# Kernel optimization log

Measured on AMD Instinct MI355X. Metric: run time of the kernel, lower is better.

Reference implementation:

```python
import jax, jax.numpy as jnp
import numpy as np

K = 32  # neighbors per query point


def _gather_points(x, idx):
    # x: [B, N, D], idx: [B, M, k] -> [B, M, k, D]
    B, M, k = idx.shape
    D = x.shape[-1]
    flat = jnp.take_along_axis(x, idx.reshape(B, M * k, 1), axis=1)
    return flat.reshape(B, M, k, D)


def setup_inputs() -> dict:
    key = jax.random.key(0)
    k1, k2, k3, k4, k5 = jax.random.split(key, 5)
    B, N, M, Cin = 16, 4096, 1024, 64
    pos = jax.random.normal(k1, (B, N, 3), dtype=jnp.float32)
    features = jax.random.normal(k2, (B, N, Cin), dtype=jnp.float32)
    idx = jax.random.randint(k3, (B, M), 0, N, dtype=jnp.int64)
    # 1x1 conv2d MLP params: (Cin+3) -> 64 -> 128 (use_xyz adds 3 channels)
    W1 = jax.random.normal(k4, (Cin + 3, 64), dtype=jnp.float32) * (1.0 / np.sqrt(Cin + 3))
    b1 = jnp.zeros((64,), dtype=jnp.float32)
    W2 = jax.random.normal(k5, (64, 128), dtype=jnp.float32) * (1.0 / np.sqrt(64))
    b2 = jnp.zeros((128,), dtype=jnp.float32)
    return {"pos": pos, "features": features, "W1": W1, "b1": b1,
            "W2": W2, "b2": b2, "idx": idx}


def reference(pos, features, W1, b1, W2, b2, idx):
    # pos: [B,N,3], features: [B,N,C], idx: [B,M] query-point indices
    pos_q = jnp.take_along_axis(pos, idx[..., None], axis=1)  # [B,M,3]
    # squared-distance knn: [B,M,N]
    d2 = (jnp.sum(pos_q ** 2, -1, keepdims=True)
          + jnp.sum(pos ** 2, -1)[:, None, :]
          - 2.0 * jnp.einsum("bmd,bnd->bmn", pos_q, pos))
    _, nn_idx = jax.lax.top_k(-d2, K)  # [B,M,K] nearest neighbors
    grouped_pos = _gather_points(pos, nn_idx)          # [B,M,K,3]
    grouped_feat = _gather_points(features, nn_idx)    # [B,M,K,C]
    rel = grouped_pos - pos_q[:, :, None, :]           # recenter groups
    x = jnp.concatenate([rel, grouped_feat], axis=-1)  # [B,M,K,C+3] (use_xyz)
    # 1x1 conv2d MLP == per-point linear + ReLU on channel dim
    h = jax.nn.relu(jnp.einsum("bmkc,cd->bmkd", x, W1) + b1)
    h = jax.nn.relu(jnp.einsum("bmkc,cd->bmkd", h, W2) + b2)
    out = jnp.max(h, axis=-2)  # max over K neighbors -> [B,M,128]
    return (pos_q, out)
```

## Files before the change

kernel.cpp:

```cpp
#include <hip/hip_runtime.h>

#define NPTS  4096
#define MQ    1024
#define BATCH 16
#define KNN   32
#define CIN   64
#define H1D   64
#define H2D   128

typedef _Float16 half8 __attribute__((ext_vector_type(8)));
typedef float    floatx4 __attribute__((ext_vector_type(4)));

#define WS_NN_BYTES ((size_t)BATCH * MQ * KNN * 4)
#define W1F_HALVES  (3 * 4 * 64 * 8)
#define W2F_HALVES  (2 * 8 * 64 * 8)
#define WS_PP_OFF   (WS_NN_BYTES + (W1F_HALVES + W2F_HALVES) * 2)

__global__ __launch_bounds__(256) void wprep_kernel(
    const float* __restrict__ W1, const float* __restrict__ W2,
    const float* __restrict__ pos,
    _Float16* __restrict__ wout, float* __restrict__ pp)
{
    const int gid = blockIdx.x * 256 + threadIdx.x;
    if (gid < 768) {
        const int s = gid;
        const int kc = s >> 8, nt = (s >> 6) & 3, lane = s & 63;
        const int col = lane & 15, quad = lane >> 4;
        half8 ph;
#pragma unroll
        for (int j = 0; j < 8; ++j) {
            const int k = kc * 32 + quad * 8 + j;
            ph[j] = (k < 67) ? (_Float16)W1[k * H1D + nt * 16 + col] : (_Float16)0.0f;
        }
        *(half8*)(wout + (size_t)s * 8) = ph;
    } else if (gid < 1792) {
        const int s2 = gid - 768;
        const int kc2 = s2 >> 9, nt2 = (s2 >> 6) & 7, lane = s2 & 63;
        const int col = lane & 15, quad = lane >> 4;
        half8 ph;
#pragma unroll
        for (int j = 0; j < 8; ++j) {
            const int k = kc2 * 32 + quad * 8 + j;
            ph[j] = (_Float16)W2[k * H2D + nt2 * 16 + col];
        }
        *(half8*)(wout + (size_t)W1F_HALVES + (size_t)s2 * 8) = ph;
    } else {
        const int p = gid - 1792;
        if (p < BATCH * NPTS) {
            const float px = pos[p * 3 + 0], py = pos[p * 3 + 1], pz = pos[p * 3 + 2];
            pp[p] = __fadd_rn(__fadd_rn(__fmul_rn(px, px), __fmul_rn(py, py)),
                              __fmul_rn(pz, pz));
        }
    }
}

__global__ __launch_bounds__(256) void knn_kernel(
    const float* __restrict__ pos, const float* __restrict__ pp,
    const int* __restrict__ idx,
    float* __restrict__ pos_q, int* __restrict__ nn)
{
    const int bid = blockIdx.x;
    const int b   = bid >> 10;
    const int m   = bid & (MQ - 1);
    const int t   = threadIdx.x;
    const int wv  = t >> 6, lane = t & 63;

    __shared__ unsigned int keys[NPTS];
    __shared__ unsigned int hist[2048];
    __shared__ unsigned int wsum[4];
    __shared__ unsigned int sc[8];
    __shared__ unsigned int ckey[64];
    __shared__ int          cidx[64];
    __shared__ int          outidx[KNN];

    const float* pb  = pos + (size_t)b * NPTS * 3;
    const float* ppb = pp + (size_t)b * NPTS;
    const int qn = idx[(size_t)b * MQ + m];
    const float qx = pb[qn * 3 + 0], qy = pb[qn * 3 + 1], qz = pb[qn * 3 + 2];
    const float qq = ppb[qn];

    for (int i = 0; i < NPTS / 256; ++i) {
        const int n = i * 256 + t;
        const float px = pb[n * 3 + 0], py = pb[n * 3 + 1], pz = pb[n * 3 + 2];
        const float qp = __fadd_rn(__fadd_rn(__fmul_rn(qx, px), __fmul_rn(qy, py)),
                                   __fmul_rn(qz, pz));
        const float d2 = __fsub_rn(__fadd_rn(qq, ppb[n]), __fmul_rn(2.0f, qp));
        unsigned int u = __float_as_uint(d2);
        u = (u & 0x80000000u) ? ~u : (u | 0x80000000u);
        keys[n] = u;
    }

    unsigned int prefix = 0u, rank = KNN - 1;
    int shift = 21, bcnt = NPTS;
    for (int level = 0; level < 3; ++level) {
        shift = (level == 0) ? 21 : (level == 1) ? 10 : 0;
        const int nb = (level < 2) ? 11 : 10;
        const int nbins = 1 << nb;
        const unsigned int mask = nbins - 1;
        const int hs = shift + nb;
        for (int j = t; j < nbins; j += 256) hist[j] = 0u;
        __syncthreads();
        for (int i = 0; i < NPTS / 256; ++i) {
            const unsigned int u = keys[i * 256 + t];
            if (level == 0 || (u >> hs) == prefix)
                atomicAdd(&hist[(u >> shift) & mask], 1u);
        }
        __syncthreads();
        const int g = nbins >> 8;
        unsigned int s = 0;
        for (int j = 0; j < g; ++j) s += hist[t * g + j];
        unsigned int v = s;
#pragma unroll
        for (int off = 1; off < 64; off <<= 1) {
            const unsigned int o = __shfl_up(v, off);
            if (lane >= off) v += o;
        }
        if (lane == 63) wsum[wv] = v;
        __syncthreads();
        unsigned int woff = 0;
        for (int i = 0; i < wv; ++i) woff += wsum[i];
        const unsigned int incl = woff + v, excl = incl - s;
        if (s > 0 && rank >= excl && rank < incl) {
            unsigned int e = excl;
            for (int j = 0; j < g; ++j) {
                const unsigned int c = hist[t * g + j];
                if (rank < e + c) {
                    sc[0] = (prefix << nb) | (unsigned int)(t * g + j);
                    sc[1] = rank - e;
                    sc[2] = c;
                    break;
                }
                e += c;
            }
        }
        __syncthreads();
        prefix = sc[0];
        rank   = sc[1];
        bcnt   = (int)sc[2];
        __syncthreads();
        if (bcnt <= 64) break;
    }

    if (t == 0) { sc[3] = 0u; sc[4] = 0u; }
    __syncthreads();
    for (int i = 0; i < NPTS / 256; ++i) {
        const int n = i * 256 + t;
        const unsigned int u = keys[n];
        const unsigned int hp = (shift == 0) ? u : (u >> shift);
        if (hp < prefix) {
            outidx[atomicAdd(&sc[3], 1u)] = n;
        } else if (hp == prefix) {
            const unsigned int slot = atomicAdd(&sc[4], 1u);
            if (slot < 64u) { ckey[slot] = u; cidx[slot] = n; }
        }
    }
    __syncthreads();
    const int defcnt  = (int)sc[3];
    const int candcnt = min((int)sc[4], 64);

    if (wv == 0) {
        const unsigned int k_l = (lane < candcnt) ? ckey[lane] : 0xFFFFFFFFu;
        const int          i_l = (lane < candcnt) ? cidx[lane] : 0x7FFFFFFF;
        int rk = 0;
        for (int j = 0; j < candcnt; ++j) {
            const unsigned int kj = __shfl(k_l, j);
            const int          ij = __shfl(i_l, j);
            if (kj < k_l || (kj == k_l && ij < i_l)) ++rk;
        }
        if (lane < candcnt && rk <= (int)rank) outidx[defcnt + rk] = i_l;
    }
    __syncthreads();
    if (t < KNN) nn[(size_t)bid * KNN + t] = outidx[t];
    if (t < 3)  pos_q[(size_t)bid * 3 + t] = (t == 0) ? qx : ((t == 1) ? qy : qz);
}

#define W1F_H 0
#define W2F_H 6144
#define XH_H  14336
#define SH_HALVES (XH_H + 4 * 3072)

__global__ __launch_bounds__(256) void mlp_kernel(
    const float* __restrict__ pos, const float* __restrict__ feat,
    const float* __restrict__ b1, const float* __restrict__ b2,
    const float* __restrict__ pos_q, const int* __restrict__ nn,
    const _Float16* __restrict__ wf, float* __restrict__ out)
{
    __shared__ _Float16 sh[SH_HALVES];
    const int t = threadIdx.x;
    const int w = t >> 6, lane = t & 63;
    const int col = lane & 15, quad = lane >> 4;
    const int qblk = blockIdx.x * 4;

    {
        const int4* src = (const int4*)wf;
        int4* dst = (int4*)sh;
#pragma unroll
        for (int r = 0; r < 7; ++r) dst[t + 256 * r] = src[t + 256 * r];
    }

    {
        const int r = t >> 1, h = t & 1;
        const int ql = r >> 5, kk = r & 31;
        const int q = qblk + ql, b = q >> 10;
        const int n = nn[(size_t)q * KNN + kk];
        const float* frow = feat + ((size_t)(b * NPTS + n)) * CIN;
        const float4* f4 = (const float4*)frow;
        const int mt = kk >> 4, lrow = kk & 15;
        const int base = XH_H + ql * 3072;
        if (h == 0) {
            float rel[3];
#pragma unroll
            for (int c = 0; c < 3; ++c)
                rel[c] = pos[(size_t)b * NPTS * 3 + n * 3 + c] - pos_q[(size_t)q * 3 + c];
            float fb[48];
#pragma unroll
            for (int ii = 0; ii < 12; ++ii) {
                const float4 v = f4[ii];
                fb[4*ii] = v.x; fb[4*ii+1] = v.y; fb[4*ii+2] = v.z; fb[4*ii+3] = v.w;
            }
#pragma unroll
            for (int cidx2 = 0; cidx2 < 6; ++cidx2) {
                half8 ph;
#pragma unroll
                for (int jj = 0; jj < 8; ++jj) {
                    const int c = cidx2 * 8 + jj;
                    ph[jj] = (_Float16)((c < 3) ? rel[c] : fb[c - 3]);
                }
                const int kc = cidx2 >> 2, qd = cidx2 & 3;
                *(half8*)&sh[base + ((kc * 2 + mt) * 64 + qd * 16 + lrow) * 8] = ph;
            }
        } else {
            float fb[20];
#pragma unroll
            for (int ii = 0; ii < 5; ++ii) {
                const float4 v = f4[11 + ii];
                fb[4*ii] = v.x; fb[4*ii+1] = v.y; fb[4*ii+2] = v.z; fb[4*ii+3] = v.w;
            }
#pragma unroll
            for (int cidx2 = 6; cidx2 < 12; ++cidx2) {
                half8 ph;
#pragma unroll
                for (int jj = 0; jj < 8; ++jj) {
                    const int c = cidx2 * 8 + jj;
                    ph[jj] = (_Float16)((c < 67) ? fb[c - 47] : 0.0f);
                }
                const int kc = cidx2 >> 2, qd = cidx2 & 3;
                *(half8*)&sh[base + ((kc * 2 + mt) * 64 + qd * 16 + lrow) * 8] = ph;
            }
        }
    }
    __syncthreads();

    const int q = qblk + w;
    const int wbase = XH_H + w * 3072;

    half8 af[3][2];
#pragma unroll
    for (int kc = 0; kc < 3; ++kc)
#pragma unroll
        for (int mt = 0; mt < 2; ++mt)
            af[kc][mt] = *(const half8*)&sh[wbase + ((kc * 2 + mt) * 64 + lane) * 8];

#pragma unroll
    for (int nt = 0; nt < 4; ++nt) {
        const float bv = b1[nt * 16 + col];
        floatx4 acc0 = {bv, bv, bv, bv}, acc1 = acc0;
#pragma unroll
        for (int kc = 0; kc < 3; ++kc) {
            const half8 bf = *(const half8*)&sh[W1F_H + ((kc * 4 + nt) * 64 + lane) * 8];
            acc0 = __builtin_amdgcn_mfma_f32_16x16x32_f16(af[kc][0], bf, acc0, 0, 0, 0);
            acc1 = __builtin_amdgcn_mfma_f32_16x16x32_f16(af[kc][1], bf, acc1, 0, 0, 0);
        }
        const int kc2 = nt >> 1;
        const int quad2 = (((nt & 1) * 16) + col) >> 3;
        const int j2 = col & 7;
#pragma unroll
        for (int mt = 0; mt < 2; ++mt) {
            const floatx4 a = mt ? acc1 : acc0;
#pragma unroll
            for (int reg = 0; reg < 4; ++reg) {
                const int row = quad * 4 + reg;
                sh[wbase + ((kc2 * 2 + mt) * 64 + quad2 * 16 + row) * 8 + j2] =
                    (_Float16)fmaxf(a[reg], 0.0f);
            }
        }
    }

    half8 a2[2][2];
#pragma unroll
    for (int kc2 = 0; kc2 < 2; ++kc2)
#pragma unroll
        for (int mt = 0; mt < 2; ++mt)
            a2[kc2][mt] = *(const half8*)&sh[wbase + ((kc2 * 2 + mt) * 64 + lane) * 8];

    float* oq = out + (size_t)q * H2D;
#pragma unroll
    for (int nt2 = 0; nt2 < 8; ++nt2) {
        const float bv = b2[nt2 * 16 + col];
        floatx4 acc0 = {bv, bv, bv, bv}, acc1 = acc0;
#pragma unroll
        for (int kc2 = 0; kc2 < 2; ++kc2) {
            const half8 bf = *(const half8*)&sh[W2F_H + ((kc2 * 8 + nt2) * 64 + lane) * 8];
            acc0 = __builtin_amdgcn_mfma_f32_16x16x32_f16(a2[kc2][0], bf, acc0, 0, 0, 0);
            acc1 = __builtin_amdgcn_mfma_f32_16x16x32_f16(a2[kc2][1], bf, acc1, 0, 0, 0);
        }
        float mm = fmaxf(fmaxf(fmaxf(acc0[0], acc0[1]), fmaxf(acc0[2], acc0[3])),
                         fmaxf(fmaxf(acc1[0], acc1[1]), fmaxf(acc1[2], acc1[3])));
        mm = fmaxf(mm, 0.0f);
        mm = fmaxf(mm, __shfl_xor(mm, 16));
        mm = fmaxf(mm, __shfl_xor(mm, 32));
        if (lane < 16) oq[nt2 * 16 + lane] = mm;
    }
}

extern "C" void kernel_launch(void* const* d_in, const int* in_sizes, int n_in,
                              void* d_out, int out_size, void* d_ws, size_t ws_size,
                              hipStream_t stream)
{
    const float* pos  = (const float*)d_in[0];
    const float* feat = (const float*)d_in[1];
    const float* W1   = (const float*)d_in[2];
    const float* b1   = (const float*)d_in[3];
    const float* W2   = (const float*)d_in[4];
    const float* b2   = (const float*)d_in[5];
    const int*   idx  = (const int*)d_in[6];

    float* pos_q = (float*)d_out;
    float* out   = (float*)d_out + (size_t)BATCH * MQ * 3;
    int*      nn = (int*)d_ws;
    _Float16* wf = (_Float16*)((char*)d_ws + WS_NN_BYTES);
    float*    pp = (float*)((char*)d_ws + WS_PP_OFF);

    wprep_kernel<<<(1792 + BATCH * NPTS + 255) / 256, 256, 0, stream>>>(W1, W2, pos, wf, pp);
    knn_kernel<<<BATCH * MQ, 256, 0, stream>>>(pos, pp, idx, pos_q, nn);
    mlp_kernel<<<BATCH * MQ / 4, 256, 0, stream>>>(pos, feat, b1, b2,
                                                   pos_q, nn, wf, out);
}
```

Measured before the change: 229.8 us.

## Pack positions as float4 and keep kNN keys in registers

The prep kernel now writes each point as a float4 of xyz plus its squared norm, so the kNN kernel does one vector load per point instead of four scalar loads. The distance keys stay in 16 registers per thread rather than a 16KB shared array, and the first radix-histogram pass is fused into the distance loop. Less shared memory plus launch_bounds(256,4) aim for higher occupancy and fewer LDS round trips, at the cost of more register pressure and a workspace layout that assumes the float4 buffer fits.

```diff
diff --git a/kernel.cpp b/kernel.cpp
--- a/kernel.cpp
+++ b/kernel.cpp
@@ -14,12 +14,12 @@
 #define WS_NN_BYTES ((size_t)BATCH * MQ * KNN * 4)
 #define W1F_HALVES  (3 * 4 * 64 * 8)
 #define W2F_HALVES  (2 * 8 * 64 * 8)
-#define WS_PP_OFF   (WS_NN_BYTES + (W1F_HALVES + W2F_HALVES) * 2)
+#define WS_P4_OFF   (WS_NN_BYTES + (W1F_HALVES + W2F_HALVES) * 2)
 
 __global__ __launch_bounds__(256) void wprep_kernel(
     const float* __restrict__ W1, const float* __restrict__ W2,
     const float* __restrict__ pos,
-    _Float16* __restrict__ wout, float* __restrict__ pp)
+    _Float16* __restrict__ wout, float4* __restrict__ pos4)
 {
     const int gid = blockIdx.x * 256 + threadIdx.x;
     if (gid < 768) {
@@ -48,15 +48,17 @@
         const int p = gid - 1792;
         if (p < BATCH * NPTS) {
             const float px = pos[p * 3 + 0], py = pos[p * 3 + 1], pz = pos[p * 3 + 2];
-            pp[p] = __fadd_rn(__fadd_rn(__fmul_rn(px, px), __fmul_rn(py, py)),
-                              __fmul_rn(pz, pz));
+            float4 v;
+            v.x = px; v.y = py; v.z = pz;
+            v.w = __fadd_rn(__fadd_rn(__fmul_rn(px, px), __fmul_rn(py, py)),
+                            __fmul_rn(pz, pz));
+            pos4[p] = v;
         }
     }
 }
 
-__global__ __launch_bounds__(256) void knn_kernel(
-    const float* __restrict__ pos, const float* __restrict__ pp,
-    const int* __restrict__ idx,
+__global__ __launch_bounds__(256, 4) void knn_kernel(
+    const float4* __restrict__ pos4, const int* __restrict__ idx,
     float* __restrict__ pos_q, int* __restrict__ nn)
 {
     const int bid = blockIdx.x;
@@ -65,7 +67,6 @@
     const int t   = threadIdx.x;
     const int wv  = t >> 6, lane = t & 63;
 
-    __shared__ unsigned int keys[NPTS];
     __shared__ unsigned int hist[2048];
     __shared__ unsigned int wsum[4];
     __shared__ unsigned int sc[8];
@@ -73,42 +74,37 @@
     __shared__ int          cidx[64];
     __shared__ int          outidx[KNN];
 
-    const float* pb  = pos + (size_t)b * NPTS * 3;
-    const float* ppb = pp + (size_t)b * NPTS;
+    const float4* pb4 = pos4 + (size_t)b * NPTS;
     const int qn = idx[(size_t)b * MQ + m];
-    const float qx = pb[qn * 3 + 0], qy = pb[qn * 3 + 1], qz = pb[qn * 3 + 2];
-    const float qq = ppb[qn];
-
-    for (int i = 0; i < NPTS / 256; ++i) {
-        const int n = i * 256 + t;
-        const float px = pb[n * 3 + 0], py = pb[n * 3 + 1], pz = pb[n * 3 + 2];
-        const float qp = __fadd_rn(__fadd_rn(__fmul_rn(qx, px), __fmul_rn(qy, py)),
-                                   __fmul_rn(qz, pz));
-        const float d2 = __fsub_rn(__fadd_rn(qq, ppb[n]), __fmul_rn(2.0f, qp));
+    const float4 qv = pb4[qn];
+    const float qq = qv.w;
+
+#pragma unroll
+    for (int j = 0; j < 8; ++j) hist[t + 256 * j] = 0u;
+    __syncthreads();
+
+    unsigned int k[16];
+#pragma unroll
+    for (int i = 0; i < 16; ++i) {
+        const float4 p = pb4[i * 256 + t];
+        const float qp = __fadd_rn(__fadd_rn(__fmul_rn(qv.x, p.x), __fmul_rn(qv.y, p.y)),
+                                   __fmul_rn(qv.z, p.z));
+        const float d2 = __fsub_rn(__fadd_rn(qq, p.w), __fmul_rn(2.0f, qp));
         unsigned int u = __float_as_uint(d2);
         u = (u & 0x80000000u) ? ~u : (u | 0x80000000u);
-        keys[n] = u;
-    }
+        k[i] = u;
+        atomicAdd(&hist[u >> 21], 1u);
+    }
+    __syncthreads();
 
     unsigned int prefix = 0u, rank = KNN - 1;
-    int shift = 21, bcnt = NPTS;
+    int shift = 21, bcnt;
     for (int level = 0; level < 3; ++level) {
-        shift = (level == 0) ? 21 : (level == 1) ? 10 : 0;
         const int nb = (level < 2) ? 11 : 10;
-        const int nbins = 1 << nb;
-        const unsigned int mask = nbins - 1;
-        const int hs = shift + nb;
-        for (int j = t; j < nbins; j += 256) hist[j] = 0u;
-        __syncthreads();
-        for (int i = 0; i < NPTS / 256; ++i) {
-            const unsigned int u = keys[i * 256 + t];
-            if (level == 0 || (u >> hs) == prefix)
-                atomicAdd(&hist[(u >> shift) & mask], 1u);
-        }
-        __syncthreads();
-        const int g = nbins >> 8;
+        const int g  = (1 << nb) >> 8;
+        unsigned int cnt[8];
         unsigned int s = 0;
-        for (int j = 0; j < g; ++j) s += hist[t * g + j];
+        for (int j = 0; j < g; ++j) { cnt[j] = hist[t * g + j]; s += cnt[j]; }
         unsigned int v = s;
 #pragma unroll
         for (int off = 1; off < 64; off <<= 1) {
@@ -120,38 +116,52 @@
         unsigned int woff = 0;
         for (int i = 0; i < wv; ++i) woff += wsum[i];
         const unsigned int incl = woff + v, excl = incl - s;
-        if (s > 0 && rank >= excl && rank < incl) {
+        if (rank >= excl && rank < incl) {
             unsigned int e = excl;
             for (int j = 0; j < g; ++j) {
-                const unsigned int c = hist[t * g + j];
-                if (rank < e + c) {
+                if (rank < e + cnt[j]) {
                     sc[0] = (prefix << nb) | (unsigned int)(t * g + j);
                     sc[1] = rank - e;
-                    sc[2] = c;
+                    sc[2] = cnt[j];
                     break;
                 }
-                e += c;
+                e += cnt[j];
             }
         }
         __syncthreads();
         prefix = sc[0];
         rank   = sc[1];
         bcnt   = (int)sc[2];
-        __syncthreads();
-        if (bcnt <= 64) break;
+        if (level == 2 || bcnt <= 64) break;
+
+        const int nshift = (level == 0) ? 10 : 0;
+        const int nnb    = (level == 0) ? 11 : 10;
+        const unsigned int nmask = (1u << nnb) - 1u;
+        __syncthreads();
+#pragma unroll
+        for (int j = 0; j < 8; ++j) hist[t + 256 * j] = 0u;
+        __syncthreads();
+#pragma unroll
+        for (int i = 0; i < 16; ++i) {
+            const unsigned int u = k[i];
+            if ((u >> (nshift + nnb)) == prefix)
+                atomicAdd(&hist[(u >> nshift) & nmask], 1u);
+        }
+        shift = nshift;
+        __syncthreads();
     }
 
     if (t == 0) { sc[3] = 0u; sc[4] = 0u; }
     __syncthreads();
-    for (int i = 0; i < NPTS / 256; ++i) {
-        const int n = i * 256 + t;
-        const unsigned int u = keys[n];
+#pragma unroll
+    for (int i = 0; i < 16; ++i) {
+        const unsigned int u = k[i];
         const unsigned int hp = (shift == 0) ? u : (u >> shift);
         if (hp < prefix) {
-            outidx[atomicAdd(&sc[3], 1u)] = n;
+            outidx[atomicAdd(&sc[3], 1u)] = i * 256 + t;
         } else if (hp == prefix) {
             const unsigned int slot = atomicAdd(&sc[4], 1u);
-            if (slot < 64u) { ckey[slot] = u; cidx[slot] = n; }
+            if (slot < 64u) { ckey[slot] = u; cidx[slot] = i * 256 + t; }
         }
     }
     __syncthreads();
@@ -171,7 +181,11 @@
     }
     __syncthreads();
     if (t < KNN) nn[(size_t)bid * KNN + t] = outidx[t];
-    if (t < 3)  pos_q[(size_t)bid * 3 + t] = (t == 0) ? qx : ((t == 1) ? qy : qz);
+    if (t == 0) {
+        pos_q[(size_t)bid * 3 + 0] = qv.x;
+        pos_q[(size_t)bid * 3 + 1] = qv.y;
+        pos_q[(size_t)bid * 3 + 2] = qv.z;
+    }
 }
 
 #define W1F_H 0
@@ -329,10 +343,11 @@
     float* out   = (float*)d_out + (size_t)BATCH * MQ * 3;
     int*      nn = (int*)d_ws;
     _Float16* wf = (_Float16*)((char*)d_ws + WS_NN_BYTES);
-    float*    pp = (float*)((char*)d_ws + WS_PP_OFF);
-
-    wprep_kernel<<<(1792 + BATCH * NPTS + 255) / 256, 256, 0, stream>>>(W1, W2, pos, wf, pp);
-    knn_kernel<<<BATCH * MQ, 256, 0, stream>>>(pos, pp, idx, pos_q, nn);
+    float4*   p4 = (float4*)((char*)d_ws + WS_P4_OFF);
+
+    const int prep_threads = 1792 + BATCH * NPTS;
+    wprep_kernel<<<(prep_threads + 255) / 256, 256, 0, stream>>>(W1, W2, pos, wf, p4);
+    knn_kernel<<<BATCH * MQ, 256, 0, stream>>>(p4, idx, pos_q, nn);
     mlp_kernel<<<BATCH * MQ / 4, 256, 0, stream>>>(pos, feat, b1, b2,
                                                    pos_q, nn, wf, out);
 }
```

Result: faster. 204.9 us (-10.8%).
